# Kernel optimization log

Measured on AMD Instinct MI355X. Metric: run time of the kernel, lower is better.

## Reference

```python
import jax, jax.numpy as jnp
import numpy as np

N = 100000
E = 1600000
IN_CH, HID_CH, OUT_CH, HEADS = 128, 32, 64, 4
NEG_SLOPE = 0.2


def gat_conv(x, src, dst, W, att_src, att_dst, bias, concat):
    """PyG-style GATConv (inference; dropout off). src/dst include self-loops.
    x: [N, Fin], W: [Fin, H*C], att_*: [H, C], bias: [H*C] or [C]."""
    n = x.shape[0]
    H, C = att_src.shape
    h = (x @ W).reshape(n, H, C)                      # [N, H, C]
    a_s = jnp.sum(h * att_src, axis=-1)               # [N, H]
    a_d = jnp.sum(h * att_dst, axis=-1)               # [N, H]
    e = jax.nn.leaky_relu(a_s[src] + a_d[dst], NEG_SLOPE)   # [E, H]
    # segment softmax over incoming edges of each dst node
    e_max = jax.ops.segment_max(e, dst, num_segments=n)     # [N, H]
    e_exp = jnp.exp(e - e_max[dst])                          # [E, H]
    denom = jax.ops.segment_sum(e_exp, dst, num_segments=n) # [N, H]
    alpha = e_exp / (denom[dst] + 1e-16)                     # [E, H]
    msg = h[src] * alpha[:, :, None]                         # [E, H, C]
    out = jax.ops.segment_sum(msg, dst, num_segments=n)     # [N, H, C]
    out = out.reshape(n, H * C) if concat else out.mean(axis=1)
    return out + bias


def setup_inputs() -> dict:
    key = jax.random.key(0)
    ks = jax.random.split(key, 10)
    g = 1.0 / np.sqrt(IN_CH)
    g2 = 1.0 / np.sqrt(HID_CH * HEADS)
    return {
        "x": jax.random.normal(ks[0], (N, IN_CH), dtype=jnp.float32),
        "edge_index": jax.random.randint(ks[1], (2, E), 0, N, dtype=jnp.int64),
        "W1": jax.random.normal(ks[2], (IN_CH, HEADS * HID_CH), dtype=jnp.float32) * g,
        "att_src1": jax.random.normal(ks[3], (HEADS, HID_CH), dtype=jnp.float32) * g,
        "att_dst1": jax.random.normal(ks[4], (HEADS, HID_CH), dtype=jnp.float32) * g,
        "b1": jnp.zeros((HEADS * HID_CH,), dtype=jnp.float32),
        "W2": jax.random.normal(ks[5], (HEADS * HID_CH, OUT_CH), dtype=jnp.float32) * g2,
        "att_src2": jax.random.normal(ks[6], (1, OUT_CH), dtype=jnp.float32) * g2,
        "att_dst2": jax.random.normal(ks[7], (1, OUT_CH), dtype=jnp.float32) * g2,
        "b2": jnp.zeros((OUT_CH,), dtype=jnp.float32),
    }


def reference(x, edge_index, W1, att_src1, att_dst1, b1, W2, att_src2, att_dst2, b2):
    n = x.shape[0]
    # GATConv adds self-loops by default (fixed-size concat: jit friendly)
    loops = jnp.arange(n, dtype=edge_index.dtype)
    src = jnp.concatenate([edge_index[0], loops])
    dst = jnp.concatenate([edge_index[1], loops])
    h = gat_conv(x, src, dst, W1, att_src1, att_dst1, b1, concat=True)
    h = jax.nn.elu(h)
    return gat_conv(h, src, dst, W2, att_src2, att_dst2, b2, concat=False)
```

## Files before the change

### kernel.cpp

```cpp
#include <hip/hip_runtime.h>
#include <hip/hip_fp16.h>

#define NEG_SLOPE 0.2f
#define BKN 128
#define MAXNB 1024
#define GRP 256

typedef _Float16 half_t;
typedef __attribute__((ext_vector_type(4))) _Float16 half4;
typedef __attribute__((ext_vector_type(8))) _Float16 half8;
typedef __attribute__((ext_vector_type(4))) float floatx4;

__global__ __launch_bounds__(256) void w_convert2(
    const float* __restrict__ W1, half_t* __restrict__ Wt1,
    const float* __restrict__ W2, half_t* __restrict__ Wt2)
{
    int i = blockIdx.x * 256 + threadIdx.x;
    if (i < 128 * 128) {
        int k = i / 128, nn = i % 128;
        Wt1[nn * 128 + k] = (half_t)W1[i];
    } else if (i < 128 * 128 + 128 * 64) {
        int j = i - 128 * 128;
        int k = j / 64, nn = j % 64;
        Wt2[nn * 128 + k] = (half_t)W2[j];
    }
}

template<int BN, int HEADS, bool INHALF>
__global__ __launch_bounds__(256) void gemm_mfma(
    const void* __restrict__ Xv, const half_t* __restrict__ Wt,
    const float* __restrict__ atts, const float* __restrict__ attd,
    half_t* __restrict__ H, float* __restrict__ As, float* __restrict__ Ad,
    int n)
{
    constexpr int K  = 128;
    constexpr int NT = BN / 16;
    constexpr int TPH = NT / HEADS;

    __shared__ half_t Wl[BN * K];
    __shared__ half_t Xl[64 * K];

    const int t = threadIdx.x;
    const int wave = t >> 6, lane = t & 63;
    const int quad = lane >> 4, c = lane & 15;

    float att_s[NT], att_d[NT];
    #pragma unroll
    for (int nt = 0; nt < NT; ++nt) {
        att_s[nt] = atts[nt * 16 + c];
        att_d[nt] = attd[nt * 16 + c];
    }

    for (int i = t; i < BN * 16; i += 256) {
        int row = i >> 4, cid = i & 15;
        half8 v = *(const half8*)(Wt + row * K + cid * 8);
        *(half8*)(Wl + row * K + ((cid ^ (row & 15)) << 3)) = v;
    }

    const int numTiles = (n + 63) / 64;
    for (int tile = blockIdx.x; tile < numTiles; tile += gridDim.x) {
        const int row0 = tile * 64;
        __syncthreads();
        for (int i = t; i < 1024; i += 256) {
            int m = i >> 4, cid = i & 15;
            int row = row0 + m;
            half8 h;
            #pragma unroll
            for (int z = 0; z < 8; ++z) h[z] = (half_t)0.f;
            if (row < n) {
                if constexpr (INHALF) {
                    h = *(const half8*)((const half_t*)Xv + (size_t)row * K + cid * 8);
                } else {
                    const float4* src = (const float4*)((const float*)Xv + (size_t)row * K + cid * 8);
                    float4 a = src[0], b = src[1];
                    h[0]=(half_t)a.x; h[1]=(half_t)a.y; h[2]=(half_t)a.z; h[3]=(half_t)a.w;
                    h[4]=(half_t)b.x; h[5]=(half_t)b.y; h[6]=(half_t)b.z; h[7]=(half_t)b.w;
                }
            }
            *(half8*)(Xl + m * K + ((cid ^ (m & 15)) << 3)) = h;
        }
        __syncthreads();

        floatx4 acc[NT];
        #pragma unroll
        for (int i = 0; i < NT; ++i) acc[i] = (floatx4)(0.f);

        #pragma unroll
        for (int kc = 0; kc < 4; ++kc) {
            int cid = kc * 4 + quad;
            half8 afrag = *(const half8*)(Xl + (wave * 16 + c) * K + ((cid ^ c) << 3));
            #pragma unroll
            for (int nt = 0; nt < NT; ++nt) {
                half8 bfrag = *(const half8*)(Wl + (nt * 16 + c) * K + ((cid ^ c) << 3));
                acc[nt] = __builtin_amdgcn_mfma_f32_16x16x32_f16(afrag, bfrag, acc[nt], 0, 0, 0);
            }
        }

        #pragma unroll
        for (int reg = 0; reg < 4; ++reg) {
            int row = row0 + wave * 16 + quad * 4 + reg;
            bool ok = row < n;
            if (ok) {
                #pragma unroll
                for (int nt = 0; nt < NT; ++nt)
                    H[(size_t)row * BN + nt * 16 + c] = (half_t)acc[nt][reg];
            }
            #pragma unroll
            for (int h = 0; h < HEADS; ++h) {
                float ps = 0.f, pd = 0.f;
                #pragma unroll
                for (int u = 0; u < TPH; ++u) {
                    int nt = h * TPH + u;
                    ps += acc[nt][reg] * att_s[nt];
                    pd += acc[nt][reg] * att_d[nt];
                }
                #pragma unroll
                for (int off = 1; off < 16; off <<= 1) {
                    ps += __shfl_xor(ps, off);
                    pd += __shfl_xor(pd, off);
                }
                if (ok && c == 0) {
                    As[(size_t)row * HEADS + h] = ps;
                    Ad[(size_t)row * HEADS + h] = pd;
                }
            }
        }
    }
}

__global__ __launch_bounds__(256) void ghist(
    const int* __restrict__ ei, int E, int Etot, int NB, int chunk,
    int* __restrict__ cnt)
{
    __shared__ int h[MAXNB];
    int g = blockIdx.x;
    for (int i = threadIdx.x; i < NB; i += 256) h[i] = 0;
    __syncthreads();
    int lo = g * chunk, hi = min(Etot, lo + chunk);
    for (int e = lo + threadIdx.x; e < hi; e += 256) {
        int dst = (e < E) ? ei[E + e] : (e - E);
        atomicAdd(&h[dst >> 7], 1);
    }
    __syncthreads();
    for (int i = threadIdx.x; i < NB; i += 256) cnt[i * GRP + g] = h[i];
}

__global__ __launch_bounds__(256) void scan_blocks(
    int* __restrict__ data, int n, int* __restrict__ bsum)
{
    __shared__ int s[256];
    int t = threadIdx.x;
    int idx = blockIdx.x * 1024 + t * 4;
    int4 v = make_int4(0, 0, 0, 0);
    if (idx + 3 < n)      v = *(const int4*)(data + idx);
    else {
        if (idx     < n) v.x = data[idx];
        if (idx + 1 < n) v.y = data[idx+1];
        if (idx + 2 < n) v.z = data[idx+2];
        if (idx + 3 < n) v.w = data[idx+3];
    }
    int tsum = v.x + v.y + v.z + v.w;
    s[t] = tsum;
    __syncthreads();
    for (int off = 1; off < 256; off <<= 1) {
        int x = (t >= off) ? s[t - off] : 0;
        __syncthreads();
        s[t] += x;
        __syncthreads();
    }
    int excl = s[t] - tsum;
    if (t == 255) bsum[blockIdx.x] = s[255];
    if (idx     < n) data[idx]     = excl;
    if (idx + 1 < n) data[idx + 1] = excl + v.x;
    if (idx + 2 < n) data[idx + 2] = excl + v.x + v.y;
    if (idx + 3 < n) data[idx + 3] = excl + v.x + v.y + v.z;
}

__global__ __launch_bounds__(256) void scan_sums(int* __restrict__ bsum, int nb)
{
    __shared__ int s[256];
    int t = threadIdx.x;
    int v = (t < nb) ? bsum[t] : 0;
    s[t] = v;
    __syncthreads();
    for (int off = 1; off < 256; off <<= 1) {
        int x = (t >= off) ? s[t - off] : 0;
        __syncthreads();
        s[t] += x;
        __syncthreads();
    }
    if (t < nb) bsum[t] = s[t] - v;
}

__global__ __launch_bounds__(256) void scan_add(
    int* __restrict__ data, int n, const int* __restrict__ bsum)
{
    int i = blockIdx.x * 256 + threadIdx.x;
    if (i < n) data[i] += bsum[i >> 10];
}

__global__ __launch_bounds__(256) void pass1_scatter(
    const int* __restrict__ ei, int E, int Etot, int NB, int chunk,
    const int* __restrict__ S, unsigned* __restrict__ tmp)
{
    __shared__ int cur[MAXNB];
    int g = blockIdx.x;
    for (int i = threadIdx.x; i < NB; i += 256) cur[i] = S[i * GRP + g];
    __syncthreads();
    int lo = g * chunk, hi = min(Etot, lo + chunk);
    for (int e = lo + threadIdx.x; e < hi; e += 256) {
        int src, dst;
        if (e < E) { src = ei[e]; dst = ei[E + e]; }
        else       { src = dst = e - E; }
        int pos = atomicAdd(&cur[dst >> 7], 1);
        tmp[pos] = ((unsigned)src << 7) | (unsigned)(dst & (BKN - 1));
    }
}

__global__ __launch_bounds__(256) void pass2_sort(
    const unsigned* __restrict__ tmp, const int* __restrict__ S,
    int NB, int Etot,
    int* __restrict__ offs, int* __restrict__ esrc, int n)
{
    __shared__ int cnt[BKN];
    __shared__ int sc[BKN];
    __shared__ int cur[BKN];
    int bk = blockIdx.x;
    int t  = threadIdx.x;
    if (t < BKN) cnt[t] = 0;
    __syncthreads();
    int lo = S[bk * GRP];
    int hi = (bk + 1 < NB) ? S[(bk + 1) * GRP] : Etot;
    for (int i = lo + t; i < hi; i += 256)
        atomicAdd(&cnt[tmp[i] & (BKN - 1)], 1);
    __syncthreads();
    int v = (t < BKN) ? cnt[t] : 0;
    if (t < BKN) sc[t] = v;
    __syncthreads();
    for (int off = 1; off < BKN; off <<= 1) {
        int x = (t < BKN && t >= off) ? sc[t - off] : 0;
        __syncthreads();
        if (t < BKN) sc[t] += x;
        __syncthreads();
    }
    if (t < BKN) {
        int node = bk * BKN + t;
        if (node < n) offs[node] = lo + sc[t];
        cur[t] = lo + sc[t] - v;
    }
    __syncthreads();
    for (int i = lo + t; i < hi; i += 256) {
        unsigned w = tmp[i];
        int p = atomicAdd(&cur[w & (BKN - 1)], 1);
        esrc[p] = (int)(w >> 7);
    }
}

__global__ __launch_bounds__(256) void agg1(
    const int* __restrict__ offs, const int* __restrict__ esrc,
    const half8* __restrict__ H8, const float* __restrict__ As,
    const float* __restrict__ Ad, const float* __restrict__ bias,
    half_t* __restrict__ X2h, int n)
{
    int v    = (blockIdx.x * 256 + threadIdx.x) >> 6;
    int lane = threadIdx.x & 63;
    if (v >= n) return;
    int q    = lane >> 4;
    int li   = lane & 15;
    int head = li >> 2;
    int end = offs[v];
    int beg = v ? offs[v - 1] : 0;
    float adv = Ad[(size_t)v * 4 + head];
    float a[8];
    #pragma unroll
    for (int f = 0; f < 8; ++f) a[f] = 0.f;
    float den = 0.f;
    int j = beg + q;
    for (; j + 4 < end; j += 8) {
        int s0 = esrc[j], s1 = esrc[j + 4];
        float e0 = As[(size_t)s0 * 4 + head] + adv;
        float e1 = As[(size_t)s1 * 4 + head] + adv;
        half8 q0 = H8[(unsigned)s0 * 16 + li];
        half8 q1 = H8[(unsigned)s1 * 16 + li];
        e0 = e0 > 0.f ? e0 : NEG_SLOPE * e0;  float w0 = __expf(e0);
        e1 = e1 > 0.f ? e1 : NEG_SLOPE * e1;  float w1 = __expf(e1);
        #pragma unroll
        for (int f = 0; f < 8; ++f)
            a[f] += w0 * (float)q0[f] + w1 * (float)q1[f];
        den += w0 + w1;
    }
    for (; j < end; j += 4) {
        int s = esrc[j];
        float e = As[(size_t)s * 4 + head] + adv;
        half8 q0 = H8[(unsigned)s * 16 + li];
        e = e > 0.f ? e : NEG_SLOPE * e;
        float w = __expf(e);
        #pragma unroll
        for (int f = 0; f < 8; ++f) a[f] += w * (float)q0[f];
        den += w;
    }
    #pragma unroll
    for (int f = 0; f < 8; ++f) {
        a[f] += __shfl_xor(a[f], 16);
        a[f] += __shfl_xor(a[f], 32);
    }
    den += __shfl_xor(den, 16);
    den += __shfl_xor(den, 32);
    if (q == 0) {
        float inv = 1.f / (den + 1e-16f);
        float4 b0 = ((const float4*)bias)[2 * li];
        float4 b1 = ((const float4*)bias)[2 * li + 1];
        float o[8];
        o[0] = a[0] * inv + b0.x; o[1] = a[1] * inv + b0.y;
        o[2] = a[2] * inv + b0.z; o[3] = a[3] * inv + b0.w;
        o[4] = a[4] * inv + b1.x; o[5] = a[5] * inv + b1.y;
        o[6] = a[6] * inv + b1.z; o[7] = a[7] * inv + b1.w;
        half8 h;
        #pragma unroll
        for (int f = 0; f < 8; ++f) {
            float e = o[f] > 0.f ? o[f] : __expf(o[f]) - 1.f;
            h[f] = (half_t)e;
        }
        *(half8*)(X2h + (size_t)v * 128 + li * 8) = h;
    }
}

__global__ __launch_bounds__(256) void agg2(
    const int* __restrict__ offs, const int* __restrict__ esrc,
    const half8* __restrict__ H8, const float* __restrict__ As,
    const float* __restrict__ Ad, const float* __restrict__ bias,
    float* __restrict__ out, int n)
{
    int v    = (blockIdx.x * 256 + threadIdx.x) >> 6;
    int lane = threadIdx.x & 63;
    if (v >= n) return;
    int g  = lane >> 3;
    int li = lane & 7;
    int end = offs[v];
    int beg = v ? offs[v - 1] : 0;
    float adv = Ad[v];
    float a[8];
    #pragma unroll
    for (int f = 0; f < 8; ++f) a[f] = 0.f;
    float den = 0.f;
    int j = beg + g;
    for (; j + 8 < end; j += 16) {
        int s0 = esrc[j], s1 = esrc[j + 8];
        float e0 = As[s0] + adv;
        float e1 = As[s1] + adv;
        half8 q0 = H8[(unsigned)s0 * 8 + li];
        half8 q1 = H8[(unsigned)s1 * 8 + li];
        e0 = e0 > 0.f ? e0 : NEG_SLOPE * e0;  float w0 = __expf(e0);
        e1 = e1 > 0.f ? e1 : NEG_SLOPE * e1;  float w1 = __expf(e1);
        #pragma unroll
        for (int f = 0; f < 8; ++f)
            a[f] += w0 * (float)q0[f] + w1 * (float)q1[f];
        den += w0 + w1;
    }
    for (; j < end; j += 8) {
        int s = esrc[j];
        float e = As[s] + adv;
        half8 q0 = H8[(unsigned)s * 8 + li];
        e = e > 0.f ? e : NEG_SLOPE * e;
        float w = __expf(e);
        #pragma unroll
        for (int f = 0; f < 8; ++f) a[f] += w * (float)q0[f];
        den += w;
    }
    #pragma unroll
    for (int f = 0; f < 8; ++f) {
        a[f] += __shfl_xor(a[f], 8);
        a[f] += __shfl_xor(a[f], 16);
        a[f] += __shfl_xor(a[f], 32);
    }
    den += __shfl_xor(den, 8);
    den += __shfl_xor(den, 16);
    den += __shfl_xor(den, 32);
    if (lane < 8) {
        float inv = 1.f / (den + 1e-16f);
        float4 b0 = ((const float4*)bias)[2 * li];
        float4 b1 = ((const float4*)bias)[2 * li + 1];
        float4* o4 = (float4*)(out + (size_t)v * 64);
        o4[2 * li]     = make_float4(a[0] * inv + b0.x, a[1] * inv + b0.y,
                                     a[2] * inv + b0.z, a[3] * inv + b0.w);
        o4[2 * li + 1] = make_float4(a[4] * inv + b1.x, a[5] * inv + b1.y,
                                     a[6] * inv + b1.z, a[7] * inv + b1.w);
    }
}

extern "C" void kernel_launch(void* const* d_in, const int* in_sizes, int n_in,
                              void* d_out, int out_size, void* d_ws, size_t ws_size,
                              hipStream_t stream)
{
    (void)n_in; (void)out_size; (void)ws_size;
    const float* x   = (const float*)d_in[0];
    const int*   ei  = (const int*)  d_in[1];
    const float* W1  = (const float*)d_in[2];
    const float* as1 = (const float*)d_in[3];
    const float* ad1 = (const float*)d_in[4];
    const float* b1  = (const float*)d_in[5];
    const float* W2  = (const float*)d_in[6];
    const float* as2 = (const float*)d_in[7];
    const float* ad2 = (const float*)d_in[8];
    const float* b2  = (const float*)d_in[9];
    float* out = (float*)d_out;

    const int n    = in_sizes[0] / 128;
    const int E    = in_sizes[1] / 2;
    const int Etot = E + n;
    const int NB   = (n + BKN - 1) / BKN;
    const int chunk = (Etot + GRP - 1) / GRP;

    char* p = (char*)d_ws;
    half_t* Hh  = (half_t*)p; p += (size_t)n * 128 * sizeof(half_t);
    half_t* X2h = (half_t*)p; p += (size_t)n * 128 * sizeof(half_t);
    float* As1 = (float*)p;   p += (size_t)n * 4 * sizeof(float);
    float* Ad1 = (float*)p;   p += (size_t)n * 4 * sizeof(float);
    int* offs  = (int*)p;     p += (size_t)n * sizeof(int);
    int* esrc  = (int*)p;     p += (size_t)Etot * sizeof(int);
    unsigned* tmp = (unsigned*)p; p += (size_t)Etot * sizeof(unsigned);
    int* cnt   = (int*)p;     p += (size_t)NB * GRP * sizeof(int);
    int* bsum  = (int*)p;     p += 1024;
    half_t* Wt1 = (half_t*)p; p += 128 * 128 * sizeof(half_t);
    half_t* Wt2 = (half_t*)p; p += 64 * 128 * sizeof(half_t);

    const int scan_n  = NB * GRP;
    const int scan_nb = (scan_n + 1023) / 1024;

    w_convert2<<<(128 * 192 + 255) / 256, 256, 0, stream>>>(W1, Wt1, W2, Wt2);

    ghist<<<GRP, 256, 0, stream>>>(ei, E, Etot, NB, chunk, cnt);
    scan_blocks<<<scan_nb, 256, 0, stream>>>(cnt, scan_n, bsum);
    scan_sums<<<1, 256, 0, stream>>>(bsum, scan_nb);
    scan_add<<<(scan_n + 255) / 256, 256, 0, stream>>>(cnt, scan_n, bsum);
    pass1_scatter<<<GRP, 256, 0, stream>>>(ei, E, Etot, NB, chunk, cnt, tmp);
    pass2_sort<<<NB, 256, 0, stream>>>(tmp, cnt, NB, Etot, offs, esrc, n);

    const int gtiles = (n + 63) / 64;

    gemm_mfma<128, 4, false><<<gtiles, 256, 0, stream>>>(x, Wt1, as1, ad1, Hh, As1, Ad1, n);
    agg1<<<(n * 64 + 255) / 256, 256, 0, stream>>>(offs, esrc, (const half8*)Hh, As1, Ad1, b1, X2h, n);

    gemm_mfma<64, 1, true><<<gtiles, 256, 0, stream>>>(X2h, Wt2, as2, ad2, Hh, As1, Ad1, n);
    agg2<<<(n * 64 + 255) / 256, 256, 0, stream>>>(offs, esrc, (const half8*)Hh, As1, Ad1, b2, out, n);
}
```

Measured before the change: 322.4 us.

## Use exp2 with prescaled attention, fp16 dot2 accumulation, 4-edge unroll, fold scan_add

Multiplies the attention vectors by log2(e) in the GEMM so the aggregation kernels can call the hardware exp2 directly, and replaces the leaky-relu branch with a fmax. The aggregation loops are unrolled to four edges per iteration and accumulate with packed fp16 dot2 instructions instead of per-element fp32 FMAs. The separate scan_add launch is removed by adding the block offsets inside pass1_scatter and pass2_sort. Rounding the softmax weights to fp16 before accumulation loses precision and can overflow for large scores, since no max subtraction is done.

Result: no change. 320.7 us (-0.5%).

```diff
diff --git a/kernel.cpp b/kernel.cpp
--- a/kernel.cpp
+++ b/kernel.cpp
@@ -5,11 +5,19 @@
 #define BKN 128
 #define MAXNB 1024
 #define GRP 256
+#define LOG2E 1.44269504f
 
 typedef _Float16 half_t;
+typedef __attribute__((ext_vector_type(2))) _Float16 half2v;
 typedef __attribute__((ext_vector_type(4))) _Float16 half4;
 typedef __attribute__((ext_vector_type(8))) _Float16 half8;
 typedef __attribute__((ext_vector_type(4))) float floatx4;
+
+#if __has_builtin(__builtin_amdgcn_fdot2)
+#define FDOT2(a, b, c) __builtin_amdgcn_fdot2((a), (b), (c), false)
+#else
+#define FDOT2(a, b, c) ((float)(a)[0] * (float)(b)[0] + (float)(a)[1] * (float)(b)[1] + (c))
+#endif
 
 __global__ __launch_bounds__(256) void w_convert2(
     const float* __restrict__ W1, half_t* __restrict__ Wt1,
@@ -47,8 +55,8 @@
     float att_s[NT], att_d[NT];
     #pragma unroll
     for (int nt = 0; nt < NT; ++nt) {
-        att_s[nt] = atts[nt * 16 + c];
-        att_d[nt] = attd[nt * 16 + c];
+        att_s[nt] = atts[nt * 16 + c] * LOG2E;
+        att_d[nt] = attd[nt * 16 + c] * LOG2E;
     }
 
     for (int i = t; i < BN * 16; i += 256) {
@@ -192,20 +200,17 @@
     if (t < nb) bsum[t] = s[t] - v;
 }
 
-__global__ __launch_bounds__(256) void scan_add(
-    int* __restrict__ data, int n, const int* __restrict__ bsum)
-{
-    int i = blockIdx.x * 256 + threadIdx.x;
-    if (i < n) data[i] += bsum[i >> 10];
-}
-
 __global__ __launch_bounds__(256) void pass1_scatter(
     const int* __restrict__ ei, int E, int Etot, int NB, int chunk,
-    const int* __restrict__ S, unsigned* __restrict__ tmp)
+    const int* __restrict__ S, const int* __restrict__ bsum,
+    unsigned* __restrict__ tmp)
 {
     __shared__ int cur[MAXNB];
     int g = blockIdx.x;
-    for (int i = threadIdx.x; i < NB; i += 256) cur[i] = S[i * GRP + g];
+    for (int i = threadIdx.x; i < NB; i += 256) {
+        int idx = i * GRP + g;
+        cur[i] = S[idx] + bsum[idx >> 10];
+    }
     __syncthreads();
     int lo = g * chunk, hi = min(Etot, lo + chunk);
     for (int e = lo + threadIdx.x; e < hi; e += 256) {
@@ -219,7 +224,7 @@
 
 __global__ __launch_bounds__(256) void pass2_sort(
     const unsigned* __restrict__ tmp, const int* __restrict__ S,
-    int NB, int Etot,
+    const int* __restrict__ bsum, int NB, int Etot,
     int* __restrict__ offs, int* __restrict__ esrc, int n)
 {
     __shared__ int cnt[BKN];
@@ -229,8 +234,8 @@
     int t  = threadIdx.x;
     if (t < BKN) cnt[t] = 0;
     __syncthreads();
-    int lo = S[bk * GRP];
-    int hi = (bk + 1 < NB) ? S[(bk + 1) * GRP] : Etot;
+    int lo = S[bk * GRP] + bsum[(bk * GRP) >> 10];
+    int hi = (bk + 1 < NB) ? (S[(bk + 1) * GRP] + bsum[((bk + 1) * GRP) >> 10]) : Etot;
     for (int i = lo + t; i < hi; i += 256)
         atomicAdd(&cnt[tmp[i] & (BKN - 1)], 1);
     __syncthreads();
@@ -271,30 +276,59 @@
     int end = offs[v];
     int beg = v ? offs[v - 1] : 0;
     float adv = Ad[(size_t)v * 4 + head];
+    half2v one; one[0] = (half_t)1.f; one[1] = (half_t)1.f;
     float a[8];
     #pragma unroll
     for (int f = 0; f < 8; ++f) a[f] = 0.f;
     float den = 0.f;
     int j = beg + q;
+    for (; j + 12 < end; j += 16) {
+        int s0 = esrc[j], s1 = esrc[j + 4], s2 = esrc[j + 8], s3 = esrc[j + 12];
+        float e0 = As[(unsigned)(s0 * 4 + head)] + adv;
+        float e1 = As[(unsigned)(s1 * 4 + head)] + adv;
+        float e2 = As[(unsigned)(s2 * 4 + head)] + adv;
+        float e3 = As[(unsigned)(s3 * 4 + head)] + adv;
+        half8 q0 = H8[(unsigned)(s0 * 16 + li)];
+        half8 q1 = H8[(unsigned)(s1 * 16 + li)];
+        half8 q2 = H8[(unsigned)(s2 * 16 + li)];
+        half8 q3 = H8[(unsigned)(s3 * 16 + li)];
+        float w0 = __builtin_amdgcn_exp2f(fmaxf(e0, NEG_SLOPE * e0));
+        float w1 = __builtin_amdgcn_exp2f(fmaxf(e1, NEG_SLOPE * e1));
+        float w2 = __builtin_amdgcn_exp2f(fmaxf(e2, NEG_SLOPE * e2));
+        float w3 = __builtin_amdgcn_exp2f(fmaxf(e3, NEG_SLOPE * e3));
+        half2v wp01; wp01[0] = (half_t)w0; wp01[1] = (half_t)w1;
+        half2v wp23; wp23[0] = (half_t)w2; wp23[1] = (half_t)w3;
+        #pragma unroll
+        for (int f = 0; f < 8; ++f) {
+            half2v p01; p01[0] = q0[f]; p01[1] = q1[f];
+            half2v p23; p23[0] = q2[f]; p23[1] = q3[f];
+            a[f] = FDOT2(p01, wp01, a[f]);
+            a[f] = FDOT2(p23, wp23, a[f]);
+        }
+        den = FDOT2(wp01, one, den);
+        den = FDOT2(wp23, one, den);
+    }
     for (; j + 4 < end; j += 8) {
         int s0 = esrc[j], s1 = esrc[j + 4];
-        float e0 = As[(size_t)s0 * 4 + head] + adv;
-        float e1 = As[(size_t)s1 * 4 + head] + adv;
-        half8 q0 = H8[(unsigned)s0 * 16 + li];
-        half8 q1 = H8[(unsigned)s1 * 16 + li];
-        e0 = e0 > 0.f ? e0 : NEG_SLOPE * e0;  float w0 = __expf(e0);
-        e1 = e1 > 0.f ? e1 : NEG_SLOPE * e1;  float w1 = __expf(e1);
-        #pragma unroll
-        for (int f = 0; f < 8; ++f)
-            a[f] += w0 * (float)q0[f] + w1 * (float)q1[f];
-        den += w0 + w1;
+        float e0 = As[(unsigned)(s0 * 4 + head)] + adv;
+        float e1 = As[(unsigned)(s1 * 4 + head)] + adv;
+        half8 q0 = H8[(unsigned)(s0 * 16 + li)];
+        half8 q1 = H8[(unsigned)(s1 * 16 + li)];
+        float w0 = __builtin_amdgcn_exp2f(fmaxf(e0, NEG_SLOPE * e0));
+        float w1 = __builtin_amdgcn_exp2f(fmaxf(e1, NEG_SLOPE * e1));
+        half2v wp; wp[0] = (half_t)w0; wp[1] = (half_t)w1;
+        #pragma unroll
+        for (int f = 0; f < 8; ++f) {
+            half2v p; p[0] = q0[f]; p[1] = q1[f];
+            a[f] = FDOT2(p, wp, a[f]);
+        }
+        den = FDOT2(wp, one, den);
     }
     for (; j < end; j += 4) {
         int s = esrc[j];
-        float e = As[(size_t)s * 4 + head] + adv;
-        half8 q0 = H8[(unsigned)s * 16 + li];
-        e = e > 0.f ? e : NEG_SLOPE * e;
-        float w = __expf(e);
+        float e = As[(unsigned)(s * 4 + head)] + adv;
+        half8 q0 = H8[(unsigned)(s * 16 + li)];
+        float w = __builtin_amdgcn_exp2f(fmaxf(e, NEG_SLOPE * e));
         #pragma unroll
         for (int f = 0; f < 8; ++f) a[f] += w * (float)q0[f];
         den += w;
@@ -339,30 +373,59 @@
     int end = offs[v];
     int beg = v ? offs[v - 1] : 0;
     float adv = Ad[v];
+    half2v one; one[0] = (half_t)1.f; one[1] = (half_t)1.f;
     float a[8];
     #pragma unroll
     for (int f = 0; f < 8; ++f) a[f] = 0.f;
     float den = 0.f;
     int j = beg + g;
+    for (; j + 24 < end; j += 32) {
+        int s0 = esrc[j], s1 = esrc[j + 8], s2 = esrc[j + 16], s3 = esrc[j + 24];
+        float e0 = As[s0] + adv;
+        float e1 = As[s1] + adv;
+        float e2 = As[s2] + adv;
+        float e3 = As[s3] + adv;
+        half8 q0 = H8[(unsigned)(s0 * 8 + li)];
+        half8 q1 = H8[(unsigned)(s1 * 8 + li)];
+        half8 q2 = H8[(unsigned)(s2 * 8 + li)];
+        half8 q3 = H8[(unsigned)(s3 * 8 + li)];
+        float w0 = __builtin_amdgcn_exp2f(fmaxf(e0, NEG_SLOPE * e0));
+        float w1 = __builtin_amdgcn_exp2f(fmaxf(e1, NEG_SLOPE * e1));
+        float w2 = __builtin_amdgcn_exp2f(fmaxf(e2, NEG_SLOPE * e2));
+        float w3 = __builtin_amdgcn_exp2f(fmaxf(e3, NEG_SLOPE * e3));
+        half2v wp01; wp01[0] = (half_t)w0; wp01[1] = (half_t)w1;
+        half2v wp23; wp23[0] = (half_t)w2; wp23[1] = (half_t)w3;
+        #pragma unroll
+        for (int f = 0; f < 8; ++f) {
+            half2v p01; p01[0] = q0[f]; p01[1] = q1[f];
+            half2v p23; p23[0] = q2[f]; p23[1] = q3[f];
+            a[f] = FDOT2(p01, wp01, a[f]);
+            a[f] = FDOT2(p23, wp23, a[f]);
+        }
+        den = FDOT2(wp01, one, den);
+        den = FDOT2(wp23, one, den);
+    }
     for (; j + 8 < end; j += 16) {
         int s0 = esrc[j], s1 = esrc[j + 8];
         float e0 = As[s0] + adv;
         float e1 = As[s1] + adv;
-        half8 q0 = H8[(unsigned)s0 * 8 + li];
-        half8 q1 = H8[(unsigned)s1 * 8 + li];
-        e0 = e0 > 0.f ? e0 : NEG_SLOPE * e0;  float w0 = __expf(e0);
-        e1 = e1 > 0.f ? e1 : NEG_SLOPE * e1;  float w1 = __expf(e1);
-        #pragma unroll
-        for (int f = 0; f < 8; ++f)
-            a[f] += w0 * (float)q0[f] + w1 * (float)q1[f];
-        den += w0 + w1;
+        half8 q0 = H8[(unsigned)(s0 * 8 + li)];
+        half8 q1 = H8[(unsigned)(s1 * 8 + li)];
+        float w0 = __builtin_amdgcn_exp2f(fmaxf(e0, NEG_SLOPE * e0));
+        float w1 = __builtin_amdgcn_exp2f(fmaxf(e1, NEG_SLOPE * e1));
+        half2v wp; wp[0] = (half_t)w0; wp[1] = (half_t)w1;
+        #pragma unroll
+        for (int f = 0; f < 8; ++f) {
+            half2v p; p[0] = q0[f]; p[1] = q1[f];
+            a[f] = FDOT2(p, wp, a[f]);
+        }
+        den = FDOT2(wp, one, den);
     }
     for (; j < end; j += 8) {
         int s = esrc[j];
         float e = As[s] + adv;
-        half8 q0 = H8[(unsigned)s * 8 + li];
-        e = e > 0.f ? e : NEG_SLOPE * e;
-        float w = __expf(e);
+        half8 q0 = H8[(unsigned)(s * 8 + li)];
+        float w = __builtin_amdgcn_exp2f(fmaxf(e, NEG_SLOPE * e));
         #pragma unroll
         for (int f = 0; f < 8; ++f) a[f] += w * (float)q0[f];
         den += w;
@@ -432,9 +495,8 @@
     ghist<<<GRP, 256, 0, stream>>>(ei, E, Etot, NB, chunk, cnt);
     scan_blocks<<<scan_nb, 256, 0, stream>>>(cnt, scan_n, bsum);
     scan_sums<<<1, 256, 0, stream>>>(bsum, scan_nb);
-    scan_add<<<(scan_n + 255) / 256, 256, 0, stream>>>(cnt, scan_n, bsum);
-    pass1_scatter<<<GRP, 256, 0, stream>>>(ei, E, Etot, NB, chunk, cnt, tmp);
-    pass2_sort<<<NB, 256, 0, stream>>>(tmp, cnt, NB, Etot, offs, esrc, n);
+    pass1_scatter<<<GRP, 256, 0, stream>>>(ei, E, Etot, NB, chunk, cnt, bsum, tmp);
+    pass2_sort<<<NB, 256, 0, stream>>>(tmp, cnt, bsum, NB, Etot, offs, esrc, n);
 
     const int gtiles = (n + 63) / 64;
 
```

## Split head-major feature layout for aggregation, fold log2e, fuse small prep kernels

Applied to the files above, without the earlier changes.

The GEMM now writes H in 32-column group-major planes and stores attention scores head-major. Aggregation becomes one templated kernel in which each wavefront handles one (group, node) pair with 16 edge slots of 4 lanes, so the gathers per head are contiguous. The log2e factor is folded into the attention vectors so the kernel can use exp2, and the weighted sums use packed fp16 dot2. The weight-conversion kernel is merged into the histogram kernel and the scan_add pass is folded into its consumers, removing two launches. The risk is fp16 rounding of the edge weights in dot2, and the layer-2 output being split across two wavefronts per node.

Result: slower. 439.4 us (+36.3%).

```diff
diff --git a/kernel.cpp b/kernel.cpp
--- a/kernel.cpp
+++ b/kernel.cpp
@@ -5,26 +5,19 @@
 #define BKN 128
 #define MAXNB 1024
 #define GRP 256
+#define LOG2E 1.44269504f
 
 typedef _Float16 half_t;
+typedef __attribute__((ext_vector_type(2))) _Float16 half2v;
 typedef __attribute__((ext_vector_type(4))) _Float16 half4;
 typedef __attribute__((ext_vector_type(8))) _Float16 half8;
 typedef __attribute__((ext_vector_type(4))) float floatx4;
 
-__global__ __launch_bounds__(256) void w_convert2(
-    const float* __restrict__ W1, half_t* __restrict__ Wt1,
-    const float* __restrict__ W2, half_t* __restrict__ Wt2)
-{
-    int i = blockIdx.x * 256 + threadIdx.x;
-    if (i < 128 * 128) {
-        int k = i / 128, nn = i % 128;
-        Wt1[nn * 128 + k] = (half_t)W1[i];
-    } else if (i < 128 * 128 + 128 * 64) {
-        int j = i - 128 * 128;
-        int k = j / 64, nn = j % 64;
-        Wt2[nn * 128 + k] = (half_t)W2[j];
-    }
-}
+#if __has_builtin(__builtin_amdgcn_fdot2)
+#define FDOT2(a, b, c) __builtin_amdgcn_fdot2((a), (b), (c), false)
+#else
+#define FDOT2(a, b, c) ((float)(a)[0] * (float)(b)[0] + (float)(a)[1] * (float)(b)[1] + (c))
+#endif
 
 template<int BN, int HEADS, bool INHALF>
 __global__ __launch_bounds__(256) void gemm_mfma(
@@ -47,8 +40,8 @@
     float att_s[NT], att_d[NT];
     #pragma unroll
     for (int nt = 0; nt < NT; ++nt) {
-        att_s[nt] = atts[nt * 16 + c];
-        att_d[nt] = attd[nt * 16 + c];
+        att_s[nt] = atts[nt * 16 + c] * LOG2E;
+        att_d[nt] = attd[nt * 16 + c] * LOG2E;
     }
 
     for (int i = t; i < BN * 16; i += 256) {
@@ -103,7 +96,7 @@
             if (ok) {
                 #pragma unroll
                 for (int nt = 0; nt < NT; ++nt)
-                    H[(size_t)row * BN + nt * 16 + c] = (half_t)acc[nt][reg];
+                    H[((size_t)(nt >> 1) * n + row) * 32 + ((nt & 1) << 4) + c] = (half_t)acc[nt][reg];
             }
             #pragma unroll
             for (int h = 0; h < HEADS; ++h) {
@@ -120,18 +113,30 @@
                     pd += __shfl_xor(pd, off);
                 }
                 if (ok && c == 0) {
-                    As[(size_t)row * HEADS + h] = ps;
-                    Ad[(size_t)row * HEADS + h] = pd;
+                    As[(size_t)h * n + row] = ps;
+                    Ad[(size_t)h * n + row] = pd;
                 }
             }
         }
     }
 }
 
-__global__ __launch_bounds__(256) void ghist(
+__global__ __launch_bounds__(256) void ghist_wconv(
     const int* __restrict__ ei, int E, int Etot, int NB, int chunk,
-    int* __restrict__ cnt)
-{
+    int* __restrict__ cnt,
+    const float* __restrict__ W1, half_t* __restrict__ Wt1,
+    const float* __restrict__ W2, half_t* __restrict__ Wt2)
+{
+    int iw = blockIdx.x * 256 + threadIdx.x;
+    if (iw < 128 * 128) {
+        int k = iw / 128, nn = iw % 128;
+        Wt1[nn * 128 + k] = (half_t)W1[iw];
+    } else if (iw < 128 * 128 + 128 * 64) {
+        int jx = iw - 128 * 128;
+        int k = jx / 64, nn = jx % 64;
+        Wt2[nn * 128 + k] = (half_t)W2[jx];
+    }
+
     __shared__ int h[MAXNB];
     int g = blockIdx.x;
     for (int i = threadIdx.x; i < NB; i += 256) h[i] = 0;
@@ -192,20 +197,17 @@
     if (t < nb) bsum[t] = s[t] - v;
 }
 
-__global__ __launch_bounds__(256) void scan_add(
-    int* __restrict__ data, int n, const int* __restrict__ bsum)
-{
-    int i = blockIdx.x * 256 + threadIdx.x;
-    if (i < n) data[i] += bsum[i >> 10];
-}
-
 __global__ __launch_bounds__(256) void pass1_scatter(
     const int* __restrict__ ei, int E, int Etot, int NB, int chunk,
-    const int* __restrict__ S, unsigned* __restrict__ tmp)
+    const int* __restrict__ S, const int* __restrict__ bsum,
+    unsigned* __restrict__ tmp)
 {
     __shared__ int cur[MAXNB];
     int g = blockIdx.x;
-    for (int i = threadIdx.x; i < NB; i += 256) cur[i] = S[i * GRP + g];
+    for (int i = threadIdx.x; i < NB; i += 256) {
+        int idx = i * GRP + g;
+        cur[i] = S[idx] + bsum[idx >> 10];
+    }
     __syncthreads();
     int lo = g * chunk, hi = min(Etot, lo + chunk);
     for (int e = lo + threadIdx.x; e < hi; e += 256) {
@@ -219,7 +221,7 @@
 
 __global__ __launch_bounds__(256) void pass2_sort(
     const unsigned* __restrict__ tmp, const int* __restrict__ S,
-    int NB, int Etot,
+    const int* __restrict__ bsum, int NB, int Etot,
     int* __restrict__ offs, int* __restrict__ esrc, int n)
 {
     __shared__ int cnt[BKN];
@@ -229,8 +231,8 @@
     int t  = threadIdx.x;
     if (t < BKN) cnt[t] = 0;
     __syncthreads();
-    int lo = S[bk * GRP];
-    int hi = (bk + 1 < NB) ? S[(bk + 1) * GRP] : Etot;
+    int lo = S[bk * GRP] + bsum[(bk * GRP) >> 10];
+    int hi = (bk + 1 < NB) ? (S[(bk + 1) * GRP] + bsum[((bk + 1) * GRP) >> 10]) : Etot;
     for (int i = lo + t; i < hi; i += 256)
         atomicAdd(&cnt[tmp[i] & (BKN - 1)], 1);
     __syncthreads();
@@ -256,135 +258,84 @@
     }
 }
 
-__global__ __launch_bounds__(256) void agg1(
+template<int NG, bool L1>
+__global__ __launch_bounds__(256) void agg_h(
     const int* __restrict__ offs, const int* __restrict__ esrc,
-    const half8* __restrict__ H8, const float* __restrict__ As,
+    const half8* __restrict__ H, const float* __restrict__ As,
     const float* __restrict__ Ad, const float* __restrict__ bias,
-    half_t* __restrict__ X2h, int n)
-{
-    int v    = (blockIdx.x * 256 + threadIdx.x) >> 6;
+    void* __restrict__ outp, int n)
+{
+    int idx  = blockIdx.x * 4 + (threadIdx.x >> 6);
     int lane = threadIdx.x & 63;
-    if (v >= n) return;
-    int q    = lane >> 4;
-    int li   = lane & 15;
-    int head = li >> 2;
+    if (idx >= n * NG) return;
+    int g = idx / n;
+    int v = idx - g * n;
+    int li   = lane & 3;
+    int slot = lane >> 2;
     int end = offs[v];
     int beg = v ? offs[v - 1] : 0;
-    float adv = Ad[(size_t)v * 4 + head];
+    const float* Asg = L1 ? (As + (size_t)g * n) : As;
+    float adv = L1 ? Ad[(size_t)g * n + v] : Ad[v];
+    const half8* Hg = H + (size_t)g * n * 4;
+    half2v one; one[0] = (half_t)1.f; one[1] = (half_t)1.f;
     float a[8];
     #pragma unroll
     for (int f = 0; f < 8; ++f) a[f] = 0.f;
     float den = 0.f;
-    int j = beg + q;
-    for (; j + 4 < end; j += 8) {
-        int s0 = esrc[j], s1 = esrc[j + 4];
-        float e0 = As[(size_t)s0 * 4 + head] + adv;
-        float e1 = As[(size_t)s1 * 4 + head] + adv;
-        half8 q0 = H8[(unsigned)s0 * 16 + li];
-        half8 q1 = H8[(unsigned)s1 * 16 + li];
-        e0 = e0 > 0.f ? e0 : NEG_SLOPE * e0;  float w0 = __expf(e0);
-        e1 = e1 > 0.f ? e1 : NEG_SLOPE * e1;  float w1 = __expf(e1);
-        #pragma unroll
-        for (int f = 0; f < 8; ++f)
-            a[f] += w0 * (float)q0[f] + w1 * (float)q1[f];
-        den += w0 + w1;
-    }
-    for (; j < end; j += 4) {
+    int j = beg + slot;
+    for (; j + 16 < end; j += 32) {
+        int s0 = esrc[j], s1 = esrc[j + 16];
+        float e0 = Asg[s0] + adv;
+        float e1 = Asg[s1] + adv;
+        half8 q0 = Hg[(unsigned)s0 * 4 + li];
+        half8 q1 = Hg[(unsigned)s1 * 4 + li];
+        float w0 = __builtin_amdgcn_exp2f(fmaxf(e0, NEG_SLOPE * e0));
+        float w1 = __builtin_amdgcn_exp2f(fmaxf(e1, NEG_SLOPE * e1));
+        half2v wp; wp[0] = (half_t)w0; wp[1] = (half_t)w1;
+        #pragma unroll
+        for (int f = 0; f < 8; ++f) {
+            half2v p; p[0] = q0[f]; p[1] = q1[f];
+            a[f] = FDOT2(p, wp, a[f]);
+        }
+        den = FDOT2(wp, one, den);
+    }
+    for (; j < end; j += 16) {
         int s = esrc[j];
-        float e = As[(size_t)s * 4 + head] + adv;
-        half8 q0 = H8[(unsigned)s * 16 + li];
-        e = e > 0.f ? e : NEG_SLOPE * e;
-        float w = __expf(e);
-        #pragma unroll
-        for (int f = 0; f < 8; ++f) a[f] += w * (float)q0[f];
+        float e = Asg[s] + adv;
+        half8 q = Hg[(unsigned)s * 4 + li];
+        float w = __builtin_amdgcn_exp2f(fmaxf(e, NEG_SLOPE * e));
+        #pragma unroll
+        for (int f = 0; f < 8; ++f) a[f] += w * (float)q[f];
         den += w;
     }
     #pragma unroll
-    for (int f = 0; f < 8; ++f) {
-        a[f] += __shfl_xor(a[f], 16);
-        a[f] += __shfl_xor(a[f], 32);
-    }
-    den += __shfl_xor(den, 16);
-    den += __shfl_xor(den, 32);
-    if (q == 0) {
+    for (int off = 4; off <= 32; off <<= 1) {
+        #pragma unroll
+        for (int f = 0; f < 8; ++f) a[f] += __shfl_xor(a[f], off);
+        den += __shfl_xor(den, off);
+    }
+    if (slot == 0) {
         float inv = 1.f / (den + 1e-16f);
-        float4 b0 = ((const float4*)bias)[2 * li];
-        float4 b1 = ((const float4*)bias)[2 * li + 1];
+        const float4* b4 = (const float4*)(bias + g * 32);
+        float4 b0 = b4[2 * li], b1 = b4[2 * li + 1];
         float o[8];
         o[0] = a[0] * inv + b0.x; o[1] = a[1] * inv + b0.y;
         o[2] = a[2] * inv + b0.z; o[3] = a[3] * inv + b0.w;
         o[4] = a[4] * inv + b1.x; o[5] = a[5] * inv + b1.y;
         o[6] = a[6] * inv + b1.z; o[7] = a[7] * inv + b1.w;
-        half8 h;
-        #pragma unroll
-        for (int f = 0; f < 8; ++f) {
-            float e = o[f] > 0.f ? o[f] : __expf(o[f]) - 1.f;
-            h[f] = (half_t)e;
-        }
-        *(half8*)(X2h + (size_t)v * 128 + li * 8) = h;
-    }
-}
-
-__global__ __launch_bounds__(256) void agg2(
-    const int* __restrict__ offs, const int* __restrict__ esrc,
-    const half8* __restrict__ H8, const float* __restrict__ As,
-    const float* __restrict__ Ad, const float* __restrict__ bias,
-    float* __restrict__ out, int n)
-{
-    int v    = (blockIdx.x * 256 + threadIdx.x) >> 6;
-    int lane = threadIdx.x & 63;
-    if (v >= n) return;
-    int g  = lane >> 3;
-    int li = lane & 7;
-    int end = offs[v];
-    int beg = v ? offs[v - 1] : 0;
-    float adv = Ad[v];
-    float a[8];
-    #pragma unroll
-    for (int f = 0; f < 8; ++f) a[f] = 0.f;
-    float den = 0.f;
-    int j = beg + g;
-    for (; j + 8 < end; j += 16) {
-        int s0 = esrc[j], s1 = esrc[j + 8];
-        float e0 = As[s0] + adv;
-        float e1 = As[s1] + adv;
-        half8 q0 = H8[(unsigned)s0 * 8 + li];
-        half8 q1 = H8[(unsigned)s1 * 8 + li];
-        e0 = e0 > 0.f ? e0 : NEG_SLOPE * e0;  float w0 = __expf(e0);
-        e1 = e1 > 0.f ? e1 : NEG_SLOPE * e1;  float w1 = __expf(e1);
-        #pragma unroll
-        for (int f = 0; f < 8; ++f)
-            a[f] += w0 * (float)q0[f] + w1 * (float)q1[f];
-        den += w0 + w1;
-    }
-    for (; j < end; j += 8) {
-        int s = esrc[j];
-        float e = As[s] + adv;
-        half8 q0 = H8[(unsigned)s * 8 + li];
-        e = e > 0.f ? e : NEG_SLOPE * e;
-        float w = __expf(e);
-        #pragma unroll
-        for (int f = 0; f < 8; ++f) a[f] += w * (float)q0[f];
-        den += w;
-    }
-    #pragma unroll
-    for (int f = 0; f < 8; ++f) {
-        a[f] += __shfl_xor(a[f], 8);
-        a[f] += __shfl_xor(a[f], 16);
-        a[f] += __shfl_xor(a[f], 32);
-    }
-    den += __shfl_xor(den, 8);
-    den += __shfl_xor(den, 16);
-    den += __shfl_xor(den, 32);
-    if (lane < 8) {
-        float inv = 1.f / (den + 1e-16f);
-        float4 b0 = ((const float4*)bias)[2 * li];
-        float4 b1 = ((const float4*)bias)[2 * li + 1];
-        float4* o4 = (float4*)(out + (size_t)v * 64);
-        o4[2 * li]     = make_float4(a[0] * inv + b0.x, a[1] * inv + b0.y,
-                                     a[2] * inv + b0.z, a[3] * inv + b0.w);
-        o4[2 * li + 1] = make_float4(a[4] * inv + b1.x, a[5] * inv + b1.y,
-                                     a[6] * inv + b1.z, a[7] * inv + b1.w);
+        if (L1) {
+            half8 h;
+            #pragma unroll
+            for (int f = 0; f < 8; ++f) {
+                float e = o[f] > 0.f ? o[f] : __expf(o[f]) - 1.f;
+                h[f] = (half_t)e;
+            }
+            *(half8*)((half_t*)outp + (size_t)v * 128 + g * 32 + li * 8) = h;
+        } else {
+            float4* o4 = (float4*)((float*)outp + (size_t)v * 64 + g * 32 + li * 8);
+            o4[0] = make_float4(o[0], o[1], o[2], o[3]);
+            o4[1] = make_float4(o[4], o[5], o[6], o[7]);
+        }
     }
 }
 
@@ -427,20 +378,17 @@
     const int scan_n  = NB * GRP;
     const int scan_nb = (scan_n + 1023) / 1024;
 
-    w_convert2<<<(128 * 192 + 255) / 256, 256, 0, stream>>>(W1, Wt1, W2, Wt2);
-
-    ghist<<<GRP, 256, 0, stream>>>(ei, E, Etot, NB, chunk, cnt);
+    ghist_wconv<<<GRP, 256, 0, stream>>>(ei, E, Etot, NB, chunk, cnt, W1, Wt1, W2, Wt2);
     scan_blocks<<<scan_nb, 256, 0, stream>>>(cnt, scan_n, bsum);
     scan_sums<<<1, 256, 0, stream>>>(bsum, scan_nb);
-    scan_add<<<(scan_n + 255) / 256, 256, 0, stream>>>(cnt, scan_n, bsum);
-    pass1_scatter<<<GRP, 256, 0, stream>>>(ei, E, Etot, NB, chunk, cnt, tmp);
-    pass2_sort<<<NB, 256, 0, stream>>>(tmp, cnt, NB, Etot, offs, esrc, n);
+    pass1_scatter<<<GRP, 256, 0, stream>>>(ei, E, Etot, NB, chunk, cnt, bsum, tmp);
+    pass2_sort<<<NB, 256, 0, stream>>>(tmp, cnt, bsum, NB, Etot, offs, esrc, n);
 
     const int gtiles = (n + 63) / 64;
 
     gemm_mfma<128, 4, false><<<gtiles, 256, 0, stream>>>(x, Wt1, as1, ad1, Hh, As1, Ad1, n);
-    agg1<<<(n * 64 + 255) / 256, 256, 0, stream>>>(offs, esrc, (const half8*)Hh, As1, Ad1, b1, X2h, n);
+    agg_h<4, true><<<(n * 4 + 3) / 4, 256, 0, stream>>>(offs, esrc, (const half8*)Hh, As1, Ad1, b1, X2h, n);
 
     gemm_mfma<64, 1, true><<<gtiles, 256, 0, stream>>>(X2h, Wt2, as2, ad2, Hh, As1, Ad1, n);
-    agg2<<<(n * 64 + 255) / 256, 256, 0, stream>>>(offs, esrc, (const half8*)Hh, As1, Ad1, b2, out, n);
-}
+    agg_h<2, false><<<(n * 2 + 3) / 4, 256, 0, stream>>>(offs, esrc, (const half8*)Hh, As1, Ad1, b2, out, n);
+}
```
